# Performance work log

Measured on AMD Instinct MI355X. Metric: run time of the kernel, lower is better.

The kernel has to match this reference:

```python
import jax, jax.numpy as jnp
import numpy as np

HIDDEN = 160
LAYERS = 32
CLASSES = 10
IN_DIM = 784


def setup_inputs() -> dict:
    key = jax.random.key(0)
    ks = jax.random.split(key, 6)
    B = 65536
    x = jax.random.normal(ks[0], (B, IN_DIM), dtype=jnp.float32)
    # embed: torch nn.Linear(IN_DIM, HIDDEN); store weight as [IN_DIM, HIDDEN] so y = x @ W + b
    embed_w = jax.random.normal(ks[1], (IN_DIM, HIDDEN), dtype=jnp.float32) / np.sqrt(IN_DIM)
    embed_b = jnp.zeros((HIDDEN,), dtype=jnp.float32)
    # 32 residual-layer weights, kaiming_normal (fan_in=HIDDEN, relu gain sqrt(2)) scaled by 0.1
    layer_w = jax.random.normal(ks[2], (LAYERS, HIDDEN, HIDDEN), dtype=jnp.float32) * (np.sqrt(2.0 / HIDDEN) * 0.1)
    head_w = jax.random.normal(ks[3], (HIDDEN, CLASSES), dtype=jnp.float32) / np.sqrt(HIDDEN)
    head_b = jnp.zeros((CLASSES,), dtype=jnp.float32)
    return {"x": x, "embed_w": embed_w, "embed_b": embed_b,
            "layer_w": layer_w, "head_w": head_w, "head_b": head_b}


def reference(x, embed_w, embed_b, layer_w, head_w, head_b):
    # x: [B, 784] (already flat)
    h = x @ embed_w + embed_b  # [B, H]

    def step(h, W):
        # y = relu(h @ W) + h
        return jax.nn.relu(h @ W) + h, None

    h, _ = jax.lax.scan(step, h, layer_w)  # scan over the 32 layer weights
    return h @ head_w + head_b  # [B, CLASSES]
```

## Files before the change

### kernel.cpp

```cpp
#include <hip/hip_runtime.h>
#include <cstdint>
#include <cstddef>


typedef __attribute__((ext_vector_type(8))) short bfrag8;
typedef __attribute__((ext_vector_type(4))) float facc4;

#define MFMA16(a, b, c) __builtin_amdgcn_mfma_f32_16x16x32_bf16((a), (b), (c), 0, 0, 0)

#define NIMG       38
#define IMG_ELEMS  27136
#define IMG_BYTES  54272
#define HS_ELEMS   10752

static __device__ __forceinline__ uint16_t f2bf16u(float v) {
    uint32_t u = __builtin_bit_cast(uint32_t, v);
    uint32_t r = u + 0x7FFFu + ((u >> 16) & 1u);
    return (uint16_t)(r >> 16);
}
static __device__ __forceinline__ uint32_t pack2_bf16(float lo, float hi) {
    return (uint32_t)f2bf16u(lo) | ((uint32_t)f2bf16u(hi) << 16);
}
static __device__ __forceinline__ uint32_t rtn_bits(float f) {
    return __builtin_bit_cast(uint32_t, f) + 0x8000u;
}
static __device__ __forceinline__ void gl_lds16(const void* g, void* l) {
    __builtin_amdgcn_global_load_lds(
        (const __attribute__((address_space(1))) uint32_t*)g,
        (__attribute__((address_space(3))) uint32_t*)l, 16, 0, 0);
}

__global__ __launch_bounds__(256) void resmlp_prep(
    const float* __restrict__ embed_w, const float* __restrict__ layer_w,
    const float* __restrict__ head_w, uint16_t* __restrict__ ws)
{
    int b = blockIdx.x;
    int img = b / 25, t = b % 25;
    int rt = t / 5, ct = t % 5;
    int tx = threadIdx.x & 31, ty = threadIdx.x >> 5;

    __shared__ float tile[32][33];
#pragma unroll
    for (int j = 0; j < 4; ++j) {
        int k = rt * 32 + ty + j * 8;
        int n = ct * 32 + tx;
        float v;
        if (img < 5) {
            int kg = img * 160 + k;
            v = (kg < 784) ? embed_w[(size_t)kg * 160 + n] : 0.f;
        } else if (img < 37) {
            v = layer_w[(size_t)(img - 5) * 25600 + (size_t)k * 160 + n];
        } else {
            v = (n < 10) ? head_w[k * 10 + n] : 0.f;
        }
        tile[ty + j * 8][tx] = v;
    }
    __syncthreads();
    uint16_t* dst = ws + (size_t)img * IMG_ELEMS;
#pragma unroll
    for (int j = 0; j < 4; ++j) {
        int n = ct * 32 + ty + j * 8;
        int k = rt * 32 + tx;
        dst[n * 168 + k] = f2bf16u(tile[tx][ty + j * 8]);
    }
}

__device__ __forceinline__ void stage_x(const float* __restrict__ x,
                                        uint16_t* Hs, int r0, int tid, int g)
{
    const int row = tid >> 2;
    const int kc  = g * 160;
    const float* xr = x + (size_t)(r0 + row) * 784 + kc;
#pragma unroll
    for (int j = 0; j < 10; ++j) {
        int c4 = (tid & 3) + j * 4;
        float4 v = (kc + c4 * 4 < 784) ? *(const float4*)(xr + c4 * 4)
                                       : make_float4(0.f, 0.f, 0.f, 0.f);
        uint2 u;
        u.x = pack2_bf16(v.x, v.y);
        u.y = pack2_bf16(v.z, v.w);
        *(uint2*)((char*)Hs + row * 336 + c4 * 8) = u;
    }
}

__global__ __launch_bounds__(256, 2) void resmlp_main(
    const float* __restrict__ x,
    const float* __restrict__ embed_b,
    const float* __restrict__ head_b,
    const uint16_t* __restrict__ ws,
    float* __restrict__ out)
{
    extern __shared__ __align__(16) uint16_t lds[];
    uint16_t* Hs = lds;
    uint16_t* Wb = lds + HS_ELEMS;

    const int tid  = threadIdx.x;
    const int lane = tid & 63;
    const int wave = tid >> 6;
    const int mg = wave >> 1;
    const int ng = wave & 1;
    const int q  = lane >> 4;
    const int ln = lane & 15;
    const int NB = ng * 80;
    const int r0 = blockIdx.x * 64;
    const bool oddl = (ln & 1) != 0;
    const uint32_t psel = oddl ? 0x03020706u : 0x07060302u;

    float bias[5];
#pragma unroll
    for (int nt = 0; nt < 5; ++nt) bias[nt] = embed_b[NB + nt * 16 + ln];
    const float hb = (ln < 10) ? head_b[ln] : 0.f;

    facc4 acc[2][5];
    facc4 resid[2][5];
#pragma unroll
    for (int mt = 0; mt < 2; ++mt)
#pragma unroll
        for (int nt = 0; nt < 5; ++nt) acc[mt][nt] = (facc4){0.f, 0.f, 0.f, 0.f};

    const char* wsb = (const char*)ws;
    const int lb = lane * 16;

    stage_x(x, Hs, r0, tid, 0);
#pragma unroll
    for (int i = 0; i < 14; ++i) {
        int idx = wave + i * 4;
        if (idx < 53)
            gl_lds16(wsb + idx * 1024 + lb, (char*)Wb + idx * 1024 + lb);
    }
    __syncthreads();

    const int abase = (mg * 32 + ln) * 168 + q * 8;
    const int bbase = (NB + ln) * 168 + q * 8;
    const int wb_base = (mg * 32 + q * 4 + (ln & 1)) * 336 + (NB + (ln & ~1)) * 2;

    for (int p = 0; p < 38; ++p) {
#pragma unroll
        for (int k = 0; k < 5; ++k) {
            bfrag8 a0 = *(const bfrag8*)(Hs + abase + 0 * (16 * 168) + k * 32);
            bfrag8 a1 = *(const bfrag8*)(Hs + abase + 1 * (16 * 168) + k * 32);
#pragma unroll
            for (int nt = 0; nt < 5; ++nt) {
                bfrag8 bf = *(const bfrag8*)(Wb + bbase + nt * (16 * 168) + k * 32);
                acc[0][nt] = MFMA16(a0, bf, acc[0][nt]);
                acc[1][nt] = MFMA16(a1, bf, acc[1][nt]);
            }
        }

        if (p == 37) {
            if (ng == 0) {
#pragma unroll
                for (int mt = 0; mt < 2; ++mt)
#pragma unroll
                    for (int r = 0; r < 4; ++r) {
                        int row = r0 + mg * 32 + mt * 16 + q * 4 + r;
                        if (ln < 10) out[row * 10 + ln] = acc[mt][0][r] + hb;
                    }
            }
            break;
        }

        __syncthreads();

        {
            const char* src = wsb + (size_t)(p + 1) * IMG_BYTES;
#pragma unroll
            for (int i = 0; i < 14; ++i) {
                int idx = wave + i * 4;
                if (idx < 53)
                    gl_lds16(src + idx * 1024 + lb, (char*)Wb + idx * 1024 + lb);
            }
        }

        if (p < 4) {
            stage_x(x, Hs, r0, tid, p + 1);
        } else {
            if (p == 4) {
#pragma unroll
                for (int mt = 0; mt < 2; ++mt)
#pragma unroll
                    for (int nt = 0; nt < 5; ++nt)
#pragma unroll
                        for (int r = 0; r < 4; ++r)
                            resid[mt][nt][r] = acc[mt][nt][r] + bias[nt];
            } else {
#pragma unroll
                for (int mt = 0; mt < 2; ++mt)
#pragma unroll
                    for (int nt = 0; nt < 5; ++nt)
#pragma unroll
                        for (int r = 0; r < 4; ++r)
                            resid[mt][nt][r] += fmaxf(acc[mt][nt][r], 0.f);
            }
#pragma unroll
            for (int mt = 0; mt < 2; ++mt) {
#pragma unroll
                for (int nt = 0; nt < 5; ++nt) {
                    acc[mt][nt] = (facc4){0.f, 0.f, 0.f, 0.f};
#pragma unroll
                    for (int pr = 0; pr < 2; ++pr) {
                        const int rl = pr * 2;
                        float a  = oddl ? resid[mt][nt][rl + 1] : resid[mt][nt][rl];
                        float bx = oddl ? resid[mt][nt][rl]     : resid[mt][nt][rl + 1];
                        uint32_t br = rtn_bits(bx);
                        uint32_t pb = (uint32_t)__builtin_amdgcn_mov_dpp(
                            (int)br, 0xB1, 0xF, 0xF, true);
                        uint32_t pk = __builtin_amdgcn_perm(pb, rtn_bits(a), psel);
                        *(uint32_t*)((char*)Hs + wb_base +
                                     mt * (16 * 336) + rl * 336 + nt * 32) = pk;
                    }
                }
            }
        }

        __syncthreads();
    }
}

extern "C" void kernel_launch(void* const* d_in, const int* in_sizes, int n_in,
                              void* d_out, int out_size, void* d_ws, size_t ws_size,
                              hipStream_t stream) {
    (void)in_sizes; (void)n_in; (void)out_size; (void)ws_size;
    const float* x       = (const float*)d_in[0];
    const float* embed_w = (const float*)d_in[1];
    const float* embed_b = (const float*)d_in[2];
    const float* layer_w = (const float*)d_in[3];
    const float* head_w  = (const float*)d_in[4];
    const float* head_b  = (const float*)d_in[5];
    float* out = (float*)d_out;

    uint16_t* ws = (uint16_t*)d_ws;

    const int dynLds = (HS_ELEMS + IMG_ELEMS) * 2;
    (void)hipFuncSetAttribute((const void*)resmlp_main,
                              hipFuncAttributeMaxDynamicSharedMemorySize, dynLds);

    resmlp_prep<<<950, 256, 0, stream>>>(embed_w, layer_w, head_w, ws);
    resmlp_main<<<1024, 256, dynLds, stream>>>(x, embed_b, head_b, ws, out);
}
```

Baseline: 453.4 us.

## Keep activations in registers using 32x32 MFMA with transposed weight fragments

Rewrites the main kernel so each wave owns 32 batch rows and keeps the hidden state in registers as the MFMA B operand. Weights are pre-packed into per-lane fragment order and streamed into LDS in half-image chunks, which double-buffers the weight loads across the layer's K halves. The change also swaps 16x16 for 32x32 MFMAs, removes the LDS round-trip of activations between layers, and reads x directly into registers with hardware bf16 conversion. In exchange it launches fewer, larger blocks (128 rows each), uses more registers per thread, and makes the output store pattern irregular.

```diff
diff --git a/kernel.cpp b/kernel.cpp
--- a/kernel.cpp
+++ b/kernel.cpp
@@ -4,14 +4,12 @@
 
 
 typedef __attribute__((ext_vector_type(8))) short bfrag8;
-typedef __attribute__((ext_vector_type(4))) float facc4;
-
-#define MFMA16(a, b, c) __builtin_amdgcn_mfma_f32_16x16x32_bf16((a), (b), (c), 0, 0, 0)
-
-#define NIMG       38
-#define IMG_ELEMS  27136
-#define IMG_BYTES  54272
-#define HS_ELEMS   10752
+typedef __attribute__((ext_vector_type(16))) float f32x16;
+typedef __attribute__((ext_vector_type(4))) uint32_t u32x4;
+
+#define MFMA32(a, b, c) __builtin_amdgcn_mfma_f32_32x32x16_bf16((a), (b), (c), 0, 0, 0)
+
+#define NFRAG_TOTAL 1855
 
 static __device__ __forceinline__ uint16_t f2bf16u(float v) {
     uint32_t u = __builtin_bit_cast(uint32_t, v);
@@ -21,8 +19,10 @@
 static __device__ __forceinline__ uint32_t pack2_bf16(float lo, float hi) {
     return (uint32_t)f2bf16u(lo) | ((uint32_t)f2bf16u(hi) << 16);
 }
-static __device__ __forceinline__ uint32_t rtn_bits(float f) {
-    return __builtin_bit_cast(uint32_t, f) + 0x8000u;
+static __device__ __forceinline__ uint32_t cvtpk(float lo, float hi) {
+    uint32_t r;
+    asm("v_cvt_pk_bf16_f32 %0, %1, %2" : "=v"(r) : "v"(lo), "v"(hi));
+    return r;
 }
 static __device__ __forceinline__ void gl_lds16(const void* g, void* l) {
     __builtin_amdgcn_global_load_lds(
@@ -34,52 +34,101 @@
     const float* __restrict__ embed_w, const float* __restrict__ layer_w,
     const float* __restrict__ head_w, uint16_t* __restrict__ ws)
 {
-    int b = blockIdx.x;
-    int img = b / 25, t = b % 25;
-    int rt = t / 5, ct = t % 5;
-    int tx = threadIdx.x & 31, ty = threadIdx.x >> 5;
-
-    __shared__ float tile[32][33];
-#pragma unroll
-    for (int j = 0; j < 4; ++j) {
-        int k = rt * 32 + ty + j * 8;
-        int n = ct * 32 + tx;
-        float v;
-        if (img < 5) {
-            int kg = img * 160 + k;
-            v = (kg < 784) ? embed_w[(size_t)kg * 160 + n] : 0.f;
-        } else if (img < 37) {
-            v = layer_w[(size_t)(img - 5) * 25600 + (size_t)k * 160 + n];
-        } else {
-            v = (n < 10) ? head_w[k * 10 + n] : 0.f;
-        }
-        tile[ty + j * 8][tx] = v;
-    }
-    __syncthreads();
-    uint16_t* dst = ws + (size_t)img * IMG_ELEMS;
-#pragma unroll
-    for (int j = 0; j < 4; ++j) {
-        int n = ct * 32 + ty + j * 8;
-        int k = rt * 32 + tx;
-        dst[n * 168 + k] = f2bf16u(tile[tx][ty + j * 8]);
-    }
-}
-
-__device__ __forceinline__ void stage_x(const float* __restrict__ x,
-                                        uint16_t* Hs, int r0, int tid, int g)
-{
-    const int row = tid >> 2;
-    const int kc  = g * 160;
-    const float* xr = x + (size_t)(r0 + row) * 784 + kc;
-#pragma unroll
-    for (int j = 0; j < 10; ++j) {
-        int c4 = (tid & 3) + j * 4;
-        float4 v = (kc + c4 * 4 < 784) ? *(const float4*)(xr + c4 * 4)
-                                       : make_float4(0.f, 0.f, 0.f, 0.f);
-        uint2 u;
-        u.x = pack2_bf16(v.x, v.y);
-        u.y = pack2_bf16(v.z, v.w);
-        *(uint2*)((char*)Hs + row * 336 + c4 * 8) = u;
+    const int fb = blockIdx.x * 4 + (threadIdx.x >> 6);
+    if (fb >= NFRAG_TOTAL) return;
+    const int l = threadIdx.x & 63;
+    const int h = l >> 5, m32 = l & 31;
+    float v[8];
+    if (fb < 245) {
+        const int kt = fb / 5, mt = fb % 5;
+        const int m = mt * 32 + m32;
+        const int kb = kt * 16 + h * 8;
+#pragma unroll
+        for (int j = 0; j < 8; ++j)
+            v[j] = embed_w[(size_t)(kb + j) * 160 + m];
+    } else if (fb < 1845) {
+        const int t = fb - 245, L = t / 50, r = t % 50, kt = r / 5, mt = r % 5;
+        const int m = mt * 32 + m32;
+        const float* W = layer_w + (size_t)L * 25600;
+        const int kb = 32 * (kt >> 1) + 16 * (kt & 1) + 4 * h;
+#pragma unroll
+        for (int j = 0; j < 8; ++j)
+            v[j] = W[(size_t)(kb + (j & 3) + 8 * (j >> 2)) * 160 + m];
+    } else {
+        const int kt = fb - 1845;
+        const int kb = 32 * (kt >> 1) + 16 * (kt & 1) + 4 * h;
+#pragma unroll
+        for (int j = 0; j < 8; ++j)
+            v[j] = (m32 < 10) ? head_w[(kb + (j & 3) + 8 * (j >> 2)) * 10 + m32] : 0.f;
+    }
+    u32x4 wv;
+    wv.x = pack2_bf16(v[0], v[1]);
+    wv.y = pack2_bf16(v[2], v[3]);
+    wv.z = pack2_bf16(v[4], v[5]);
+    wv.w = pack2_bf16(v[6], v[7]);
+    *(u32x4*)((char*)ws + (size_t)fb * 1024 + l * 16) = wv;
+}
+
+struct StageP { int S, C, D; };
+static __device__ __forceinline__ StageP stage_params(int u, int hf) {
+    StageP p;
+    if (u < 5)       { p.S = u * 50 + hf * 25;            p.C = (u == 4 && hf) ? 20 : 25; p.D = hf * 25600; }
+    else if (u < 37) { p.S = 245 + (u - 5) * 50 + hf * 25; p.C = 25;                      p.D = hf * 25600; }
+    else             { p.S = 1845 + hf * 5;                p.C = 5;                        p.D = hf * 5120;  }
+    return p;
+}
+
+template<int K0, int K1>
+static __device__ __forceinline__ void embed_loadx(const float* __restrict__ xb,
+                                                   float4 (&xv)[10])
+{
+#pragma unroll
+    for (int kt = K0; kt < K1; ++kt) {
+        xv[2 * (kt - K0)]     = *(const float4*)(xb + kt * 16);
+        xv[2 * (kt - K0) + 1] = *(const float4*)(xb + kt * 16 + 4);
+    }
+}
+
+template<int K0, int K1>
+static __device__ __forceinline__ void embed_mfma(const float4 (&xv)[10],
+    const uint16_t* __restrict__ lds, f32x16 (&acc)[5], int lane8)
+{
+#pragma unroll
+    for (int kt = K0; kt < K1; ++kt) {
+        const float4 v0 = xv[2 * (kt - K0)], v1 = xv[2 * (kt - K0) + 1];
+        u32x4 bw;
+        bw.x = cvtpk(v0.x, v0.y);
+        bw.y = cvtpk(v0.z, v0.w);
+        bw.z = cvtpk(v1.x, v1.y);
+        bw.w = cvtpk(v1.z, v1.w);
+        const bfrag8 b = __builtin_bit_cast(bfrag8, bw);
+#pragma unroll
+        for (int mt = 0; mt < 5; ++mt) {
+            const bfrag8 a = *(const bfrag8*)(lds + (kt * 5 + mt) * 512 + lane8);
+            acc[mt] = MFMA32(a, b, acc[mt]);
+        }
+    }
+}
+
+template<int K0, int K1, int NMT>
+static __device__ __forceinline__ void layer_mfma(
+    const uint16_t* __restrict__ lds, f32x16 (&acc)[5],
+    const f32x16 (&resid)[5], int lane8)
+{
+#pragma unroll
+    for (int kt = K0; kt < K1; ++kt) {
+        const int ms = kt >> 1, rb = (kt & 1) * 8;
+        u32x4 bw;
+        bw.x = cvtpk(resid[ms][rb + 0], resid[ms][rb + 1]);
+        bw.y = cvtpk(resid[ms][rb + 2], resid[ms][rb + 3]);
+        bw.z = cvtpk(resid[ms][rb + 4], resid[ms][rb + 5]);
+        bw.w = cvtpk(resid[ms][rb + 6], resid[ms][rb + 7]);
+        const bfrag8 b = __builtin_bit_cast(bfrag8, bw);
+#pragma unroll
+        for (int mt = 0; mt < NMT; ++mt) {
+            const bfrag8 a = *(const bfrag8*)(lds + (kt * NMT + mt) * 512 + lane8);
+            acc[mt] = MFMA32(a, b, acc[mt]);
+        }
     }
 }
 
@@ -91,129 +140,106 @@
     float* __restrict__ out)
 {
     extern __shared__ __align__(16) uint16_t lds[];
-    uint16_t* Hs = lds;
-    uint16_t* Wb = lds + HS_ELEMS;
-
     const int tid  = threadIdx.x;
-    const int lane = tid & 63;
-    const int wave = tid >> 6;
-    const int mg = wave >> 1;
-    const int ng = wave & 1;
-    const int q  = lane >> 4;
-    const int ln = lane & 15;
-    const int NB = ng * 80;
-    const int r0 = blockIdx.x * 64;
-    const bool oddl = (ln & 1) != 0;
-    const uint32_t psel = oddl ? 0x03020706u : 0x07060302u;
-
-    float bias[5];
-#pragma unroll
-    for (int nt = 0; nt < 5; ++nt) bias[nt] = embed_b[NB + nt * 16 + ln];
-    const float hb = (ln < 10) ? head_b[ln] : 0.f;
-
-    facc4 acc[2][5];
-    facc4 resid[2][5];
-#pragma unroll
-    for (int mt = 0; mt < 2; ++mt)
-#pragma unroll
-        for (int nt = 0; nt < 5; ++nt) acc[mt][nt] = (facc4){0.f, 0.f, 0.f, 0.f};
-
-    const char* wsb = (const char*)ws;
-    const int lb = lane * 16;
-
-    stage_x(x, Hs, r0, tid, 0);
-#pragma unroll
-    for (int i = 0; i < 14; ++i) {
-        int idx = wave + i * 4;
-        if (idx < 53)
-            gl_lds16(wsb + idx * 1024 + lb, (char*)Wb + idx * 1024 + lb);
-    }
+    const int wave = tid >> 6, lane = tid & 63;
+    const int hi = lane >> 5, ln = lane & 31;
+    const int lane8 = lane * 8;
+    const int batch = blockIdx.x * 128 + wave * 32 + ln;
+
+    f32x16 acc[5], resid[5];
+#pragma unroll
+    for (int mt = 0; mt < 5; ++mt)
+#pragma unroll
+        for (int r = 0; r < 16; ++r) acc[mt][r] = 0.f;
+
+    auto do_stage = [&](int u, int hf) {
+        const StageP p = stage_params(u, hf);
+        const char* src = (const char*)ws + (size_t)p.S * 1024 + lane * 16;
+        char* dst = (char*)lds + p.D + lane * 16;
+        for (int i = wave; i < p.C; i += 4)
+            gl_lds16(src + (size_t)i * 1024, dst + i * 1024);
+    };
+
+    do_stage(0, 0);
     __syncthreads();
 
-    const int abase = (mg * 32 + ln) * 168 + q * 8;
-    const int bbase = (NB + ln) * 168 + q * 8;
-    const int wb_base = (mg * 32 + q * 4 + (ln & 1)) * 336 + (NB + (ln & ~1)) * 2;
-
-    for (int p = 0; p < 38; ++p) {
-#pragma unroll
-        for (int k = 0; k < 5; ++k) {
-            bfrag8 a0 = *(const bfrag8*)(Hs + abase + 0 * (16 * 168) + k * 32);
-            bfrag8 a1 = *(const bfrag8*)(Hs + abase + 1 * (16 * 168) + k * 32);
-#pragma unroll
-            for (int nt = 0; nt < 5; ++nt) {
-                bfrag8 bf = *(const bfrag8*)(Wb + bbase + nt * (16 * 168) + k * 32);
-                acc[0][nt] = MFMA16(a0, bf, acc[0][nt]);
-                acc[1][nt] = MFMA16(a1, bf, acc[1][nt]);
-            }
-        }
-
-        if (p == 37) {
-            if (ng == 0) {
-#pragma unroll
-                for (int mt = 0; mt < 2; ++mt)
-#pragma unroll
-                    for (int r = 0; r < 4; ++r) {
-                        int row = r0 + mg * 32 + mt * 16 + q * 4 + r;
-                        if (ln < 10) out[row * 10 + ln] = acc[mt][0][r] + hb;
-                    }
-            }
-            break;
-        }
-
-        __syncthreads();
-
-        {
-            const char* src = wsb + (size_t)(p + 1) * IMG_BYTES;
-#pragma unroll
-            for (int i = 0; i < 14; ++i) {
-                int idx = wave + i * 4;
-                if (idx < 53)
-                    gl_lds16(src + idx * 1024 + lb, (char*)Wb + idx * 1024 + lb);
-            }
-        }
-
-        if (p < 4) {
-            stage_x(x, Hs, r0, tid, p + 1);
+    for (int c = 0; c < 5; ++c) {
+        const float* xb = x + (size_t)batch * 784 + c * 160 + hi * 8;
+        float4 xv[10];
+        embed_loadx<0, 5>(xb, xv);
+        do_stage(c, 1);
+        embed_mfma<0, 5>(xv, lds, acc, lane8);
+        __syncthreads();
+        if (c < 4) {
+            embed_loadx<5, 10>(xb, xv);
+            do_stage(c + 1, 0);
+            embed_mfma<5, 10>(xv, lds, acc, lane8);
         } else {
-            if (p == 4) {
-#pragma unroll
-                for (int mt = 0; mt < 2; ++mt)
-#pragma unroll
-                    for (int nt = 0; nt < 5; ++nt)
-#pragma unroll
-                        for (int r = 0; r < 4; ++r)
-                            resid[mt][nt][r] = acc[mt][nt][r] + bias[nt];
-            } else {
-#pragma unroll
-                for (int mt = 0; mt < 2; ++mt)
-#pragma unroll
-                    for (int nt = 0; nt < 5; ++nt)
-#pragma unroll
-                        for (int r = 0; r < 4; ++r)
-                            resid[mt][nt][r] += fmaxf(acc[mt][nt][r], 0.f);
-            }
-#pragma unroll
-            for (int mt = 0; mt < 2; ++mt) {
-#pragma unroll
-                for (int nt = 0; nt < 5; ++nt) {
-                    acc[mt][nt] = (facc4){0.f, 0.f, 0.f, 0.f};
-#pragma unroll
-                    for (int pr = 0; pr < 2; ++pr) {
-                        const int rl = pr * 2;
-                        float a  = oddl ? resid[mt][nt][rl + 1] : resid[mt][nt][rl];
-                        float bx = oddl ? resid[mt][nt][rl]     : resid[mt][nt][rl + 1];
-                        uint32_t br = rtn_bits(bx);
-                        uint32_t pb = (uint32_t)__builtin_amdgcn_mov_dpp(
-                            (int)br, 0xB1, 0xF, 0xF, true);
-                        uint32_t pk = __builtin_amdgcn_perm(pb, rtn_bits(a), psel);
-                        *(uint32_t*)((char*)Hs + wb_base +
-                                     mt * (16 * 336) + rl * 336 + nt * 32) = pk;
-                    }
+            embed_loadx<5, 9>(xb, xv);
+            do_stage(5, 0);
+            embed_mfma<5, 9>(xv, lds, acc, lane8);
+        }
+        __syncthreads();
+    }
+
+    for (int L = 0; L < 32; ++L) {
+        do_stage(5 + L, 1);
+        if (L == 0) {
+#pragma unroll
+            for (int mt = 0; mt < 5; ++mt)
+#pragma unroll
+                for (int q2 = 0; q2 < 4; ++q2) {
+                    const float4 b4 = *(const float4*)(embed_b + mt * 32 + q2 * 8 + hi * 4);
+                    resid[mt][q2 * 4 + 0] = acc[mt][q2 * 4 + 0] + b4.x;
+                    resid[mt][q2 * 4 + 1] = acc[mt][q2 * 4 + 1] + b4.y;
+                    resid[mt][q2 * 4 + 2] = acc[mt][q2 * 4 + 2] + b4.z;
+                    resid[mt][q2 * 4 + 3] = acc[mt][q2 * 4 + 3] + b4.w;
                 }
-            }
-        }
-
-        __syncthreads();
+        } else {
+#pragma unroll
+            for (int mt = 0; mt < 5; ++mt)
+#pragma unroll
+                for (int r = 0; r < 16; ++r)
+                    resid[mt][r] += fmaxf(acc[mt][r], 0.f);
+        }
+#pragma unroll
+        for (int mt = 0; mt < 5; ++mt)
+#pragma unroll
+            for (int r = 0; r < 16; ++r) acc[mt][r] = 0.f;
+
+        layer_mfma<0, 5, 5>(lds, acc, resid, lane8);
+        __syncthreads();
+        do_stage(L < 31 ? 6 + L : 37, 0);
+        layer_mfma<5, 10, 5>(lds, acc, resid, lane8);
+        __syncthreads();
+    }
+
+    do_stage(37, 1);
+#pragma unroll
+    for (int mt = 0; mt < 5; ++mt)
+#pragma unroll
+        for (int r = 0; r < 16; ++r)
+            resid[mt][r] += fmaxf(acc[mt][r], 0.f);
+#pragma unroll
+    for (int r = 0; r < 16; ++r) acc[0][r] = 0.f;
+
+    layer_mfma<0, 5, 1>(lds, acc, resid, lane8);
+    __syncthreads();
+    layer_mfma<5, 10, 1>(lds, acc, resid, lane8);
+
+    float* op = out + (size_t)batch * 10;
+    if (hi == 0) {
+        op[0] = acc[0][0] + head_b[0];
+        op[1] = acc[0][1] + head_b[1];
+        op[2] = acc[0][2] + head_b[2];
+        op[3] = acc[0][3] + head_b[3];
+        op[8] = acc[0][4] + head_b[8];
+        op[9] = acc[0][5] + head_b[9];
+    } else {
+        op[4] = acc[0][0] + head_b[4];
+        op[5] = acc[0][1] + head_b[5];
+        op[6] = acc[0][2] + head_b[6];
+        op[7] = acc[0][3] + head_b[7];
     }
 }
 
@@ -231,10 +257,10 @@
 
     uint16_t* ws = (uint16_t*)d_ws;
 
-    const int dynLds = (HS_ELEMS + IMG_ELEMS) * 2;
+    const int dynLds = 51200;
     (void)hipFuncSetAttribute((const void*)resmlp_main,
                               hipFuncAttributeMaxDynamicSharedMemorySize, dynLds);
 
-    resmlp_prep<<<950, 256, 0, stream>>>(embed_w, layer_w, head_w, ws);
-    resmlp_main<<<1024, 256, dynLds, stream>>>(x, embed_b, head_b, ws, out);
-}
+    resmlp_prep<<<(NFRAG_TOTAL + 3) / 4, 256, 0, stream>>>(embed_w, layer_w, head_w, ws);
+    resmlp_main<<<512, 256, dynLds, stream>>>(x, embed_b, head_b, ws, out);
+}
```

Result: faster. 397.3 us (-12.4%).
